# Kernel tuning notes

Hardware: AMD Instinct MI355X
Metric: run time of the kernel (lower is better)

Reference implementation:

```python
import jax, jax.numpy as jnp
import numpy as np

B, C, O = 8, 32, 64
G_IN, G_OUT, G_F = 33, 15, 7
X, Y, K = 64, 64, 5
INIT_ADJUST = 0.1


def setup_inputs() -> dict:
    key = jax.random.key(0)
    k1, k2, k3, k4 = jax.random.split(key, 4)
    x = jax.random.normal(k1, (B, C, G_IN, X, Y), dtype=jnp.float32)
    # idx[i, f] = in_index_dict[g_i * h_f]; per output element the G_F group
    # translates are distinct, so sample without replacement per row.
    rows = [jax.random.permutation(k, G_IN)[:G_F] for k in jax.random.split(k2, G_OUT)]
    idx = jnp.stack(rows).astype(jnp.int32)  # [G_OUT, G_F]
    weight = jax.random.normal(k3, (O, C, G_F, K, K), dtype=jnp.float32) * INIT_ADJUST
    bias = jax.random.uniform(k4, (O,), dtype=jnp.float32)
    return {"x": x, "weight": weight, "bias": bias, "idx": idx}


def reference(x, weight, bias, idx):
    # Equivalent to: scatter weight into a depth-G_IN zero kernel per output
    # group element, concat over G_OUT, run full-depth VALID conv3d.
    # Direct form: out[b,o,i,x,y] = sum_{c,f,kh,kw} x[b,c,idx[i,f],x+kh,y+kw]*W[o,c,f,kh,kw]
    b, c, g_in, xx, yy = x.shape
    o, _, g_f, kh, kw = weight.shape
    g_out = idx.shape[0]
    xg = x[:, :, idx]                                   # [B, C, G_out, G_f, X, Y]
    xg = xg.transpose(0, 2, 1, 3, 4, 5).reshape(b * g_out, c * g_f, xx, yy)
    w = weight.reshape(o, c * g_f, kh, kw)
    out = jax.lax.conv_general_dilated(
        xg, w, window_strides=(1, 1), padding="VALID",
        dimension_numbers=("NCHW", "OIHW", "NCHW"))    # [B*G_out, O, X', Y']
    out = out.reshape(b, g_out, o, xx - kh + 1, yy - kw + 1).transpose(0, 2, 1, 3, 4)
    return out + bias[None, :, None, None, None]
```

## Files before the change

kernel.cpp:

```cpp
#include <hip/hip_runtime.h>
#include <hip/hip_bf16.h>

#define B_    8
#define GOUT  15
#define GF    7
#define TAPS  25
#define CCH   224
#define NCHNK 7
#define NTILE 10
#define TROWS 6
#define SROWS 10
#define NPOS  360
#define NF_   23

typedef __attribute__((ext_vector_type(8))) __bf16 bf16x8;
typedef __attribute__((ext_vector_type(8))) unsigned short u16x8;
typedef __attribute__((ext_vector_type(4))) float f32x4;

__device__ __forceinline__ f32x4 mfma16(u16x8 a, u16x8 b, f32x4 c) {
  return __builtin_amdgcn_mfma_f32_16x16x32_bf16(
      __builtin_bit_cast(bf16x8, a), __builtin_bit_cast(bf16x8, b), c, 0, 0, 0);
}

__global__ void wt_kernel(const float* __restrict__ w, unsigned short* __restrict__ wt) {
  int i = blockIdx.x * 256 + threadIdx.x;
  if (i >= TAPS * NCHNK * 64 * 32) return;
  int e   = i & 7;
  int s   = (i >> 3) & 3;
  int o   = (i >> 5) & 63;
  int ck  = (i >> 11) % NCHNK;
  int tap = i / (NCHNK * 64 * 32);
  int cc = ck * 32 + 8 * (s ^ ((o >> 1) & 3)) + e;
  int c = cc / GF, f = cc - GF * (cc / GF);
  float v = w[(size_t)o * (32 * GF * TAPS) + c * (GF * TAPS) + f * TAPS + tap];
  __bf16 hb = (__bf16)v;
  wt[i] = __builtin_bit_cast(unsigned short, hb);
}

__global__ void __launch_bounds__(256, 2)
conv_kernel(const float* __restrict__ x, const unsigned short* __restrict__ wt,
            const float* __restrict__ bias, const int* __restrict__ idx,
            float* __restrict__ out) {
  __shared__ __align__(16) unsigned short Xs[640 * 32];
  __shared__ __align__(16) unsigned short Ws[5 * 2048];
  __shared__ float sBias[64];

  const int bid  = blockIdx.x;
  const int tile = bid % NTILE;
  const int g    = (bid / NTILE) % GOUT;
  const int b    = bid / (NTILE * GOUT);

  const int tid  = threadIdx.x;
  const int lane = tid & 63;
  const int wv   = tid >> 6;
  const int lo   = lane & 15;
  const int lk   = lane >> 4;
  const int col  = tid & 63;

  if (tid < 64) sBias[tid] = bias[tid];

  int p0[6];
  int pvalid = 0;
#pragma unroll
  for (int i = 0; i < 6; ++i) {
    int nf = wv + 4 * i;
    p0[i] = 0;
    if (nf < NF_) {
      int p = nf * 16 + lo;
      int pc = (p < NPOS) ? p : 0;
      p0[i] = (pc / 60) * 64 + (pc - 60 * (pc / 60));
      pvalid = i + 1;
    }
  }

  f32x4 acc[4][6];
#pragma unroll
  for (int m = 0; m < 4; ++m)
#pragma unroll
    for (int i = 0; i < 6; ++i) acc[m][i] = f32x4{0.f, 0.f, 0.f, 0.f};

  const unsigned short* wsrc = wt + tid * 8;
  u16x8 wr[5];
  auto wprefetch = [&](int grp) {
    int ckp = grp / 5, kh = grp - 5 * (grp / 5);
#pragma unroll
    for (int t = 0; t < 5; ++t)
      wr[t] = *reinterpret_cast<const u16x8*>(wsrc + ((kh * 5 + t) * NCHNK + ckp) * 2048);
  };

  wprefetch(0);
  const int r0 = tile * TROWS;

  for (int ck = 0; ck < NCHNK; ++ck) {
    const int c0 = ck * 32;
    int ib[8];
#pragma unroll
    for (int k = 0; k < 8; ++k) {
      int cc = c0 + 8 * wv + k;
      int c = cc / GF, f = cc - GF * c;
      int gin = idx[g * GF + f];
      ib[k] = ((b * 32 + c) * 33 + gin) * 4096;
    }

    __syncthreads();
#pragma unroll
    for (int t = 0; t < 5; ++t)
      *reinterpret_cast<u16x8*>(&Ws[t * 2048 + tid * 8]) = wr[t];
    wprefetch(ck * 5 + 1);

#pragma unroll
    for (int row = 0; row < SROWS; ++row) {
      int ga = (r0 + row) * 64 + col;
      u16x8 pk;
#pragma unroll
      for (int k = 0; k < 8; ++k) {
        float v = x[ib[k] + ga];
        pk[k] = __builtin_bit_cast(unsigned short, (__bf16)v);
      }
      int pos = row * 64 + col;
      *reinterpret_cast<u16x8*>(&Xs[pos * 32 + 8 * (wv ^ ((pos >> 1) & 3))]) = pk;
    }
    __syncthreads();

    for (int kh = 0; kh < 5; ++kh) {
      if (kh > 0) {
        __syncthreads();
#pragma unroll
        for (int t = 0; t < 5; ++t)
          *reinterpret_cast<u16x8*>(&Ws[t * 2048 + tid * 8]) = wr[t];
        int g2 = ck * 5 + kh + 1;
        if (g2 < 35) wprefetch(g2);
        __syncthreads();
      }
#pragma unroll
      for (int kw = 0; kw < 5; ++kw) {
        u16x8 a[4], bfr[6];
#pragma unroll
        for (int m = 0; m < 4; ++m)
          a[m] = *reinterpret_cast<const u16x8*>(
              &Ws[kw * 2048 + (m * 16 + lo) * 32 + 8 * (lk ^ ((lo >> 1) & 3))]);
#pragma unroll
        for (int i = 0; i < 6; ++i)
          if (i < pvalid) {
            int pt = p0[i] + kh * 64 + kw;
            bfr[i] = *reinterpret_cast<const u16x8*>(
                &Xs[pt * 32 + 8 * (lk ^ ((pt >> 1) & 3))]);
          }
#pragma unroll
        for (int i = 0; i < 6; ++i)
          if (i < pvalid)
#pragma unroll
            for (int m = 0; m < 4; ++m)
              acc[m][i] = mfma16(a[m], bfr[i], acc[m][i]);
      }
    }
  }

#pragma unroll
  for (int i = 0; i < 6; ++i) {
    if (i < pvalid) {
      int nf = wv + 4 * i;
      int p  = nf * 16 + lo;
      if (p < NPOS) {
        const size_t pb = (size_t)tile * NPOS + p;
#pragma unroll
        for (int m = 0; m < 4; ++m)
#pragma unroll
          for (int v = 0; v < 4; ++v) {
            int o = m * 16 + 4 * lk + v;
            out[(size_t)(b * 960 + o * 15 + g) * 3600 + pb] = acc[m][i][v] + sBias[o];
          }
      }
    }
  }
}

extern "C" void kernel_launch(void* const* d_in, const int* in_sizes, int n_in,
                              void* d_out, int out_size, void* d_ws, size_t ws_size,
                              hipStream_t stream) {
  const float* x      = (const float*)d_in[0];
  const float* weight = (const float*)d_in[1];
  const float* bias   = (const float*)d_in[2];
  const int*   idx    = (const int*)d_in[3];
  float* out = (float*)d_out;
  unsigned short* wt = (unsigned short*)d_ws;

  wt_kernel<<<(TAPS * NCHNK * 64 * 32 + 255) / 256, 256, 0, stream>>>(weight, wt);
  conv_kernel<<<B_ * GOUT * NTILE, 256, 0, stream>>>(x, wt, bias, idx, out);
}
```

Measured before the change: 330.6 us.

## Switch to 32x32x16 MFMA with weights streamed from global into registers

Replaces the 16x16x32 bf16 MFMA tiles with 32x32x16 tiles. Weight fragments are now loaded straight from global memory into registers with a one-tap-ahead prefetch, which removes the LDS weight staging and its extra barriers. It also raises launch bounds to 4 blocks per SM, remaps block IDs to interleave batches across XCDs, and hoists the idx lookups. In exchange each wave makes many small global weight loads that rely on cache hits, and the tighter launch bound may force register spills.

```diff
diff --git a/kernel.cpp b/kernel.cpp
--- a/kernel.cpp
+++ b/kernel.cpp
@@ -1,113 +1,100 @@
 #include <hip/hip_runtime.h>
 #include <hip/hip_bf16.h>
 
-#define B_    8
-#define GOUT  15
 #define GF    7
 #define TAPS  25
-#define CCH   224
 #define NCHNK 7
 #define NTILE 10
 #define TROWS 6
 #define SROWS 10
 #define NPOS  360
-#define NF_   23
 
-typedef __attribute__((ext_vector_type(8))) __bf16 bf16x8;
-typedef __attribute__((ext_vector_type(8))) unsigned short u16x8;
-typedef __attribute__((ext_vector_type(4))) float f32x4;
+typedef __attribute__((ext_vector_type(8)))  __bf16 bf16x8;
+typedef __attribute__((ext_vector_type(8)))  unsigned short u16x8;
+typedef __attribute__((ext_vector_type(16))) float f32x16;
 
-__device__ __forceinline__ f32x4 mfma16(u16x8 a, u16x8 b, f32x4 c) {
-  return __builtin_amdgcn_mfma_f32_16x16x32_bf16(
+__device__ __forceinline__ f32x16 mfma32(u16x8 a, u16x8 b, f32x16 c) {
+  return __builtin_amdgcn_mfma_f32_32x32x16_bf16(
       __builtin_bit_cast(bf16x8, a), __builtin_bit_cast(bf16x8, b), c, 0, 0, 0);
 }
 
 __global__ void wt_kernel(const float* __restrict__ w, unsigned short* __restrict__ wt) {
   int i = blockIdx.x * 256 + threadIdx.x;
   if (i >= TAPS * NCHNK * 64 * 32) return;
-  int e   = i & 7;
-  int s   = (i >> 3) & 3;
+  int c8  = i & 31;
   int o   = (i >> 5) & 63;
   int ck  = (i >> 11) % NCHNK;
   int tap = i / (NCHNK * 64 * 32);
-  int cc = ck * 32 + 8 * (s ^ ((o >> 1) & 3)) + e;
+  int cc = ck * 32 + c8;
   int c = cc / GF, f = cc - GF * (cc / GF);
   float v = w[(size_t)o * (32 * GF * TAPS) + c * (GF * TAPS) + f * TAPS + tap];
   __bf16 hb = (__bf16)v;
   wt[i] = __builtin_bit_cast(unsigned short, hb);
 }
 
-__global__ void __launch_bounds__(256, 2)
+__global__ void __launch_bounds__(256, 4)
 conv_kernel(const float* __restrict__ x, const unsigned short* __restrict__ wt,
             const float* __restrict__ bias, const int* __restrict__ idx,
             float* __restrict__ out) {
   __shared__ __align__(16) unsigned short Xs[640 * 32];
-  __shared__ __align__(16) unsigned short Ws[5 * 2048];
-  __shared__ float sBias[64];
 
-  const int bid  = blockIdx.x;
+  const int bid0 = blockIdx.x;
+  const int bid  = (bid0 & 7) * 150 + (bid0 >> 3);
   const int tile = bid % NTILE;
-  const int g    = (bid / NTILE) % GOUT;
-  const int b    = bid / (NTILE * GOUT);
+  const int g    = (bid / NTILE) % 15;
+  const int b    = bid / (NTILE * 15);
 
   const int tid  = threadIdx.x;
   const int lane = tid & 63;
   const int wv   = tid >> 6;
-  const int lo   = lane & 15;
-  const int lk   = lane >> 4;
+  const int l31  = lane & 31;
+  const int hi   = lane >> 5;
   const int col  = tid & 63;
 
-  if (tid < 64) sBias[tid] = bias[tid];
+  int gidx[GF];
+#pragma unroll
+  for (int f = 0; f < GF; ++f) gidx[f] = idx[g * GF + f];
 
-  int p0[6];
-  int pvalid = 0;
+  int pt0[3];
 #pragma unroll
-  for (int i = 0; i < 6; ++i) {
-    int nf = wv + 4 * i;
-    p0[i] = 0;
-    if (nf < NF_) {
-      int p = nf * 16 + lo;
-      int pc = (p < NPOS) ? p : 0;
-      p0[i] = (pc / 60) * 64 + (pc - 60 * (pc / 60));
-      pvalid = i + 1;
-    }
+  for (int i = 0; i < 3; ++i) {
+    int p  = (4 * i + wv) * 32 + l31;
+    int pc = (p < NPOS) ? p : 0;
+    int ph = pc / 60;
+    pt0[i] = ph * 64 + (pc - 60 * ph);
   }
 
-  f32x4 acc[4][6];
+  f32x16 acc[2][3];
 #pragma unroll
-  for (int m = 0; m < 4; ++m)
+  for (int m = 0; m < 2; ++m)
 #pragma unroll
-    for (int i = 0; i < 6; ++i) acc[m][i] = f32x4{0.f, 0.f, 0.f, 0.f};
+    for (int i = 0; i < 3; ++i)
+#pragma unroll
+      for (int r = 0; r < 16; ++r) acc[m][i][r] = 0.f;
 
-  const unsigned short* wsrc = wt + tid * 8;
-  u16x8 wr[5];
-  auto wprefetch = [&](int grp) {
-    int ckp = grp / 5, kh = grp - 5 * (grp / 5);
+  const int alane = l31 * 32 + hi * 8;
+  u16x8 wa[2][2], wn[2][2];
+  {
+    const unsigned short* p = wt + alane;
 #pragma unroll
-    for (int t = 0; t < 5; ++t)
-      wr[t] = *reinterpret_cast<const u16x8*>(wsrc + ((kh * 5 + t) * NCHNK + ckp) * 2048);
-  };
+    for (int m = 0; m < 2; ++m)
+#pragma unroll
+      for (int ks = 0; ks < 2; ++ks)
+        wn[m][ks] = *reinterpret_cast<const u16x8*>(p + m * 1024 + ks * 16);
+  }
 
-  wprefetch(0);
   const int r0 = tile * TROWS;
 
   for (int ck = 0; ck < NCHNK; ++ck) {
-    const int c0 = ck * 32;
     int ib[8];
 #pragma unroll
     for (int k = 0; k < 8; ++k) {
-      int cc = c0 + 8 * wv + k;
+      int cc = ck * 32 + 8 * wv + k;
       int c = cc / GF, f = cc - GF * c;
-      int gin = idx[g * GF + f];
-      ib[k] = ((b * 32 + c) * 33 + gin) * 4096;
+      ib[k] = ((b * 32 + c) * 33 + gidx[f]) * 4096;
     }
 
     __syncthreads();
-#pragma unroll
-    for (int t = 0; t < 5; ++t)
-      *reinterpret_cast<u16x8*>(&Ws[t * 2048 + tid * 8]) = wr[t];
-    wprefetch(ck * 5 + 1);
-
 #pragma unroll
     for (int row = 0; row < SROWS; ++row) {
       int ga = (r0 + row) * 64 + col;
@@ -123,54 +110,61 @@
     __syncthreads();
 
     for (int kh = 0; kh < 5; ++kh) {
-      if (kh > 0) {
-        __syncthreads();
-#pragma unroll
-        for (int t = 0; t < 5; ++t)
-          *reinterpret_cast<u16x8*>(&Ws[t * 2048 + tid * 8]) = wr[t];
-        int g2 = ck * 5 + kh + 1;
-        if (g2 < 35) wprefetch(g2);
-        __syncthreads();
-      }
 #pragma unroll
       for (int kw = 0; kw < 5; ++kw) {
-        u16x8 a[4], bfr[6];
+        const int tap = kh * 5 + kw;
 #pragma unroll
-        for (int m = 0; m < 4; ++m)
-          a[m] = *reinterpret_cast<const u16x8*>(
-              &Ws[kw * 2048 + (m * 16 + lo) * 32 + 8 * (lk ^ ((lo >> 1) & 3))]);
+        for (int m = 0; m < 2; ++m)
 #pragma unroll
-        for (int i = 0; i < 6; ++i)
-          if (i < pvalid) {
-            int pt = p0[i] + kh * 64 + kw;
-            bfr[i] = *reinterpret_cast<const u16x8*>(
-                &Xs[pt * 32 + 8 * (lk ^ ((pt >> 1) & 3))]);
+          for (int ks = 0; ks < 2; ++ks) wa[m][ks] = wn[m][ks];
+        int ntap = tap + 1, nck = ck;
+        if (ntap == TAPS) { ntap = 0; nck = (ck + 1 < NCHNK) ? ck + 1 : 0; }
+        const unsigned short* p = wt + (((ntap * NCHNK) + nck) << 11) + alane;
+#pragma unroll
+        for (int m = 0; m < 2; ++m)
+#pragma unroll
+          for (int ks = 0; ks < 2; ++ks)
+            wn[m][ks] = *reinterpret_cast<const u16x8*>(p + m * 1024 + ks * 16);
+
+        const int toff = kh * 64 + kw;
+#pragma unroll
+        for (int ks = 0; ks < 2; ++ks) {
+          u16x8 bf[3];
+#pragma unroll
+          for (int i = 0; i < 3; ++i) {
+            int pt = pt0[i] + toff;
+            bf[i] = *reinterpret_cast<const u16x8*>(
+                &Xs[pt * 32 + 8 * ((2 * ks + hi) ^ ((pt >> 1) & 3))]);
           }
 #pragma unroll
-        for (int i = 0; i < 6; ++i)
-          if (i < pvalid)
+          for (int i = 0; i < 3; ++i)
 #pragma unroll
-            for (int m = 0; m < 4; ++m)
-              acc[m][i] = mfma16(a[m], bfr[i], acc[m][i]);
+            for (int m = 0; m < 2; ++m)
+              acc[m][i] = mfma32(wa[m][ks], bf[i], acc[m][i]);
+        }
       }
     }
   }
 
+  float bv[2][16];
 #pragma unroll
-  for (int i = 0; i < 6; ++i) {
-    if (i < pvalid) {
-      int nf = wv + 4 * i;
-      int p  = nf * 16 + lo;
-      if (p < NPOS) {
-        const size_t pb = (size_t)tile * NPOS + p;
+  for (int m = 0; m < 2; ++m)
 #pragma unroll
-        for (int m = 0; m < 4; ++m)
+    for (int r = 0; r < 16; ++r)
+      bv[m][r] = bias[m * 32 + 4 * hi + (r & 3) + 8 * (r >> 2)];
+
 #pragma unroll
-          for (int v = 0; v < 4; ++v) {
-            int o = m * 16 + 4 * lk + v;
-            out[(size_t)(b * 960 + o * 15 + g) * 3600 + pb] = acc[m][i][v] + sBias[o];
-          }
-      }
+  for (int i = 0; i < 3; ++i) {
+    int p = (4 * i + wv) * 32 + l31;
+    if (p < NPOS) {
+      const size_t pb = (size_t)tile * NPOS + p;
+#pragma unroll
+      for (int m = 0; m < 2; ++m)
+#pragma unroll
+        for (int r = 0; r < 16; ++r) {
+          int o = m * 32 + 4 * hi + (r & 3) + 8 * (r >> 2);
+          out[((size_t)(b * 64 + o) * 15 + g) * 3600 + pb] = acc[m][i][r] + bv[m][r];
+        }
     }
   }
 }
@@ -186,5 +180,5 @@
   unsigned short* wt = (unsigned short*)d_ws;
 
   wt_kernel<<<(TAPS * NCHNK * 64 * 32 + 255) / 256, 256, 0, stream>>>(weight, wt);
-  conv_kernel<<<B_ * GOUT * NTILE, 256, 0, stream>>>(x, wt, bias, idx, out);
+  conv_kernel<<<8 * 15 * NTILE, 256, 0, stream>>>(x, wt, bias, idx, out);
 }
```

Result: slower. 1.005 ms (+204.0%).

## Stream weights via global_load_lds, flatten loop, and remap blocks across XCDs

Applied to the files above, without the earlier changes.

Weight tiles are now loaded straight into LDS with global_load_lds instead of being staged through registers, and the nested chunk/kh loops become a single 35-step loop with one barrier pair per step. Block IDs are permuted so that consecutive blocks are spread across the 8 XCDs. Bias is read into registers rather than shared memory, and A-fragment offsets are hoisted. This cuts register pressure and the extra LDS barriers. The trade-off is that weight loads are no longer prefetched a full step ahead: issue happens right after the trailing barrier, which may expose load latency.

```diff
diff --git a/kernel.cpp b/kernel.cpp
--- a/kernel.cpp
+++ b/kernel.cpp
@@ -1,25 +1,29 @@
 #include <hip/hip_runtime.h>
 #include <hip/hip_bf16.h>
 
-#define B_    8
-#define GOUT  15
 #define GF    7
 #define TAPS  25
-#define CCH   224
 #define NCHNK 7
 #define NTILE 10
 #define TROWS 6
 #define SROWS 10
 #define NPOS  360
 #define NF_   23
+#define NGRP  35
 
-typedef __attribute__((ext_vector_type(8))) __bf16 bf16x8;
-typedef __attribute__((ext_vector_type(8))) unsigned short u16x8;
-typedef __attribute__((ext_vector_type(4))) float f32x4;
+typedef __attribute__((ext_vector_type(8)))  __bf16 bf16x8;
+typedef __attribute__((ext_vector_type(8)))  unsigned short u16x8;
+typedef __attribute__((ext_vector_type(4)))  float f32x4;
 
 __device__ __forceinline__ f32x4 mfma16(u16x8 a, u16x8 b, f32x4 c) {
   return __builtin_amdgcn_mfma_f32_16x16x32_bf16(
       __builtin_bit_cast(bf16x8, a), __builtin_bit_cast(bf16x8, b), c, 0, 0, 0);
+}
+
+__device__ __forceinline__ void glds16(const unsigned short* g, unsigned short* l) {
+  __builtin_amdgcn_global_load_lds(
+      (__attribute__((address_space(1))) void*)g,
+      (__attribute__((address_space(3))) void*)l, 16, 0, 0);
 }
 
 __global__ void wt_kernel(const float* __restrict__ w, unsigned short* __restrict__ wt) {
@@ -43,21 +47,30 @@
             float* __restrict__ out) {
   __shared__ __align__(16) unsigned short Xs[640 * 32];
   __shared__ __align__(16) unsigned short Ws[5 * 2048];
-  __shared__ float sBias[64];
 
-  const int bid  = blockIdx.x;
+  const int bid0 = blockIdx.x;
+  const int bid  = (bid0 & 7) * 150 + (bid0 >> 3);
   const int tile = bid % NTILE;
-  const int g    = (bid / NTILE) % GOUT;
-  const int b    = bid / (NTILE * GOUT);
+  const int g    = (bid / NTILE) % 15;
+  const int b    = bid / (NTILE * 15);
 
   const int tid  = threadIdx.x;
   const int lane = tid & 63;
   const int wv   = tid >> 6;
   const int lo   = lane & 15;
   const int lk   = lane >> 4;
-  const int col  = tid & 63;
+  const int col  = lane;
 
-  if (tid < 64) sBias[tid] = bias[tid];
+  auto issue_ws = [&](int gi) {
+    const int ckp = gi / 5, khp = gi - 5 * (gi / 5);
+#pragma unroll
+    for (int t = 0; t < 5; ++t) {
+      const int tap = khp * 5 + t;
+      glds16(wt + (((size_t)(tap * NCHNK + ckp)) << 11) + tid * 8,
+             &Ws[t * 2048 + wv * 512]);
+    }
+  };
+  issue_ws(0);
 
   int p0[6];
   int pvalid = 0;
@@ -66,12 +79,18 @@
     int nf = wv + 4 * i;
     p0[i] = 0;
     if (nf < NF_) {
-      int p = nf * 16 + lo;
+      int p  = nf * 16 + lo;
       int pc = (p < NPOS) ? p : 0;
-      p0[i] = (pc / 60) * 64 + (pc - 60 * (pc / 60));
+      int ph = pc / 60;
+      p0[i] = ph * 64 + (pc - 60 * ph);
       pvalid = i + 1;
     }
   }
+
+  int aoff[4];
+#pragma unroll
+  for (int m = 0; m < 4; ++m)
+    aoff[m] = (m * 16 + lo) * 32 + 8 * (lk ^ ((lo >> 1) & 3));
 
   f32x4 acc[4][6];
 #pragma unroll
@@ -79,82 +98,64 @@
 #pragma unroll
     for (int i = 0; i < 6; ++i) acc[m][i] = f32x4{0.f, 0.f, 0.f, 0.f};
 
-  const unsigned short* wsrc = wt + tid * 8;
-  u16x8 wr[5];
-  auto wprefetch = [&](int grp) {
-    int ckp = grp / 5, kh = grp - 5 * (grp / 5);
-#pragma unroll
-    for (int t = 0; t < 5; ++t)
-      wr[t] = *reinterpret_cast<const u16x8*>(wsrc + ((kh * 5 + t) * NCHNK + ckp) * 2048);
-  };
-
-  wprefetch(0);
   const int r0 = tile * TROWS;
 
-  for (int ck = 0; ck < NCHNK; ++ck) {
-    const int c0 = ck * 32;
-    int ib[8];
-#pragma unroll
-    for (int k = 0; k < 8; ++k) {
-      int cc = c0 + 8 * wv + k;
-      int c = cc / GF, f = cc - GF * c;
-      int gin = idx[g * GF + f];
-      ib[k] = ((b * 32 + c) * 33 + gin) * 4096;
-    }
-
-    __syncthreads();
-#pragma unroll
-    for (int t = 0; t < 5; ++t)
-      *reinterpret_cast<u16x8*>(&Ws[t * 2048 + tid * 8]) = wr[t];
-    wprefetch(ck * 5 + 1);
-
-#pragma unroll
-    for (int row = 0; row < SROWS; ++row) {
-      int ga = (r0 + row) * 64 + col;
-      u16x8 pk;
+  for (int gi = 0; gi < NGRP; ++gi) {
+    const int ck = gi / 5;
+    const int kh = gi - 5 * ck;
+    if (kh == 0) {
+      int ib[8];
 #pragma unroll
       for (int k = 0; k < 8; ++k) {
-        float v = x[ib[k] + ga];
-        pk[k] = __builtin_bit_cast(unsigned short, (__bf16)v);
+        int cc = ck * 32 + 8 * wv + k;
+        int c = cc / GF, f = cc - GF * c;
+        ib[k] = ((b * 32 + c) * 33 + idx[g * GF + f]) << 12;
       }
-      int pos = row * 64 + col;
-      *reinterpret_cast<u16x8*>(&Xs[pos * 32 + 8 * (wv ^ ((pos >> 1) & 3))]) = pk;
+#pragma unroll
+      for (int row = 0; row < SROWS; ++row) {
+        int ga = (r0 + row) * 64 + col;
+        u16x8 pk;
+#pragma unroll
+        for (int k = 0; k < 8; ++k) {
+          float v = x[ib[k] + ga];
+          pk[k] = __builtin_bit_cast(unsigned short, (__bf16)v);
+        }
+        int pos = row * 64 + col;
+        *reinterpret_cast<u16x8*>(&Xs[pos * 32 + 8 * (wv ^ ((pos >> 1) & 3))]) = pk;
+      }
     }
     __syncthreads();
 
-    for (int kh = 0; kh < 5; ++kh) {
-      if (kh > 0) {
-        __syncthreads();
 #pragma unroll
-        for (int t = 0; t < 5; ++t)
-          *reinterpret_cast<u16x8*>(&Ws[t * 2048 + tid * 8]) = wr[t];
-        int g2 = ck * 5 + kh + 1;
-        if (g2 < 35) wprefetch(g2);
-        __syncthreads();
-      }
+    for (int kw = 0; kw < 5; ++kw) {
+      u16x8 a[4], bf[6];
 #pragma unroll
-      for (int kw = 0; kw < 5; ++kw) {
-        u16x8 a[4], bfr[6];
+      for (int m = 0; m < 4; ++m)
+        a[m] = *reinterpret_cast<const u16x8*>(&Ws[kw * 2048 + aoff[m]]);
+      const int toff = kh * 64 + kw;
 #pragma unroll
-        for (int m = 0; m < 4; ++m)
-          a[m] = *reinterpret_cast<const u16x8*>(
-              &Ws[kw * 2048 + (m * 16 + lo) * 32 + 8 * (lk ^ ((lo >> 1) & 3))]);
+      for (int i = 0; i < 6; ++i)
+        if (i < pvalid) {
+          int pt = p0[i] + toff;
+          bf[i] = *reinterpret_cast<const u16x8*>(
+              &Xs[pt * 32 + 8 * (lk ^ ((pt >> 1) & 3))]);
+        }
 #pragma unroll
-        for (int i = 0; i < 6; ++i)
-          if (i < pvalid) {
-            int pt = p0[i] + kh * 64 + kw;
-            bfr[i] = *reinterpret_cast<const u16x8*>(
-                &Xs[pt * 32 + 8 * (lk ^ ((pt >> 1) & 3))]);
-          }
+      for (int i = 0; i < 6; ++i)
+        if (i < pvalid)
 #pragma unroll
-        for (int i = 0; i < 6; ++i)
-          if (i < pvalid)
+          for (int m = 0; m < 4; ++m)
+            acc[m][i] = mfma16(a[m], bf[i], acc[m][i]);
+    }
+    __syncthreads();
+    if (gi + 1 < NGRP) issue_ws(gi + 1);
+  }
+
+  float bv[4][4];
 #pragma unroll
-            for (int m = 0; m < 4; ++m)
-              acc[m][i] = mfma16(a[m], bfr[i], acc[m][i]);
-      }
-    }
-  }
+  for (int m = 0; m < 4; ++m)
+#pragma unroll
+    for (int v = 0; v < 4; ++v) bv[m][v] = bias[m * 16 + 4 * lk + v];
 
 #pragma unroll
   for (int i = 0; i < 6; ++i) {
@@ -168,7 +169,7 @@
 #pragma unroll
           for (int v = 0; v < 4; ++v) {
             int o = m * 16 + 4 * lk + v;
-            out[(size_t)(b * 960 + o * 15 + g) * 3600 + pb] = acc[m][i][v] + sBias[o];
+            out[((size_t)(b * 64 + o) * 15 + g) * 3600 + pb] = acc[m][i][v] + bv[m][v];
           }
       }
     }
@@ -186,5 +187,5 @@
   unsigned short* wt = (unsigned short*)d_ws;
 
   wt_kernel<<<(TAPS * NCHNK * 64 * 32 + 255) / 256, 256, 0, stream>>>(weight, wt);
-  conv_kernel<<<B_ * GOUT * NTILE, 256, 0, stream>>>(x, wt, bias, idx, out);
+  conv_kernel<<<8 * 15 * NTILE, 256, 0, stream>>>(x, wt, bias, idx, out);
 }
```

After: 307.2 us. 1.08x faster.
